# Performance work log

Hardware: AMD Instinct MI355X
Metric: run time of the kernel (lower is better)

Reference implementation:

```python
import jax, jax.numpy as jnp
import numpy as np

H = 128  # hidden_size

def _band_agg(h):
    # Equivalent to bmm(adj, h) with adj = degree-normalized tridiagonal
    # (self + left + right neighbor), degree=3 interior, 2 at endpoints,
    # normalization adj/(deg+1e-8) as in the torch module.
    B, S, D = h.shape
    hp = jnp.pad(h, ((0, 0), (1, 1), (0, 0)))
    s = hp[:, :-2] + hp[:, 1:-1] + hp[:, 2:]            # [B,S,D] neighbor sum
    deg = jnp.full((S,), 3.0, dtype=h.dtype).at[0].set(2.0).at[S - 1].set(2.0)
    return s / (deg + 1e-8)[None, :, None]


def setup_inputs() -> dict:
    key = jax.random.key(0)
    ks = jax.random.split(key, 16)
    f32 = jnp.float32
    p = lambda k, shp: (jax.random.normal(k, shp, dtype=f32) * 0.05)
    return {
        "x": jax.random.normal(ks[0], (32, 2048, 6), dtype=f32),
        "enc_w1": p(ks[1], (6, H)),   "enc_b1": p(ks[2], (H,)),
        "enc_w2": p(ks[3], (H, H)),   "enc_b2": p(ks[4], (H,)),
        "gc1_w": p(ks[5], (H, H)),    "gc1_b": p(ks[6], (H,)),
        "gc2_w": p(ks[7], (H, H)),    "gc2_b": p(ks[8], (H,)),
        "gc3_w": p(ks[9], (H, H)),    "gc3_b": p(ks[10], (H,)),
        "cls_w1": p(ks[11], (H, H // 2)), "cls_b1": p(ks[12], (H // 2,)),
        "cls_w2": p(ks[13], (H // 2, 3)), "cls_b2": p(ks[14], (3,)),
    }


def reference(x, enc_w1, enc_b1, enc_w2, enc_b2,
              gc1_w, gc1_b, gc2_w, gc2_b, gc3_w, gc3_b,
              cls_w1, cls_b1, cls_w2, cls_b2):
    # node encoder: Linear -> ReLU -> Linear
    h = jax.nn.relu(x @ enc_w1 + enc_b1) @ enc_w2 + enc_b2
    # three graph convolutions: linear, normalized tridiagonal aggregate, relu
    h = jax.nn.relu(_band_agg(h @ gc1_w + gc1_b))
    h = jax.nn.relu(_band_agg(h @ gc2_w + gc2_b))
    h = jax.nn.relu(_band_agg(h @ gc3_w + gc3_b))
    # AdaptiveAvgPool1d(1) over seq dim after transpose == mean over nodes
    pooled = h.mean(axis=1)                              # [B, H]
    # classifier (dropout inactive in eval)
    return jax.nn.relu(pooled @ cls_w1 + cls_b1) @ cls_w2 + cls_b2
```

## Files before the change

### kernel.cpp

```cpp
#include <hip/hip_runtime.h>

#define SEQ  2048
#define HID  128
#define NB   32
#define TILE 58
#define GX   36
#define MSTR 67

typedef float f2    __attribute__((ext_vector_type(2)));
typedef float f32x4 __attribute__((ext_vector_type(4)));
typedef short bf16x8 __attribute__((ext_vector_type(8)));
typedef unsigned u32x4 __attribute__((ext_vector_type(4)));

__device__ __forceinline__ void split_bf16(float v, short& h, short& l) {
  unsigned u = __float_as_uint(v);
  unsigned r = (u + 0x7fffu + ((u >> 16) & 1u)) >> 16;
  h = (short)r;
  const float hf = __uint_as_float(r << 16);
  const float lo = v - hf;
  unsigned u2 = __float_as_uint(lo);
  unsigned r2 = (u2 + 0x7fffu + ((u2 >> 16) & 1u)) >> 16;
  l = (short)r2;
}

__device__ __forceinline__ unsigned cvt_pk_bf16(float a, float b) {
  unsigned r;
  asm("v_cvt_pk_bf16_f32 %0, %1, %2" : "=v"(r) : "v"(a), "v"(b));
  return r;
}

__global__ __launch_bounds__(256) void prep_kernel(
    const float* __restrict__ enc_w2, const float* __restrict__ enc_b2,
    const float* __restrict__ gc1_w, const float* __restrict__ gc1_b,
    const float* __restrict__ gc2_w, const float* __restrict__ gc3_w,
    short* __restrict__ Wf, float* __restrict__ bp, unsigned* __restrict__ cnt)
{
  const int tid = threadIdx.x;
  const int bid = blockIdx.x;

  if (bid == 96) {
    if (tid < 128) {
      float s = gc1_b[tid];
      for (int k = 0; k < 128; ++k) s = fmaf(enc_b2[k], gc1_w[k * 128 + tid], s);
      bp[tid] = s;
    }
    if (tid < NB) cnt[tid] = 0u;
    return;
  }

  const int L = bid >> 5, bx = bid & 31;
  short* hi = Wf + L * 32768;
  short* lo = hi + 16384;

  if (L == 0) {
    __shared__ float As[32 * 128];
    __shared__ float Bs[128 * 16];
    const int k0 = (bx >> 3) * 32, n0 = (bx & 7) * 16;
    for (int i = tid; i < 1024; i += 256)
      ((f32x4*)As)[i] = ((const f32x4*)(enc_w2 + k0 * 128))[i];
    for (int i = tid; i < 512; i += 256) {
      const int t = i >> 2, q = i & 3;
      ((f32x4*)Bs)[i] = *(const f32x4*)(gc1_w + t * 128 + n0 + q * 4);
    }
    __syncthreads();
    #pragma unroll
    for (int e = 0; e < 2; ++e) {
      const int f = tid + e * 256;
      const int l = f >> 3, j = f & 7;
      const float* ar = As + ((l >> 4) * 8 + j) * 128;
      const int nn = l & 15;
      float s0 = 0.f, s1 = 0.f, s2 = 0.f, s3 = 0.f;
      for (int t = 0; t < 128; t += 4) {
        s0 = fmaf(ar[t + 0], Bs[(t + 0) * 16 + nn], s0);
        s1 = fmaf(ar[t + 1], Bs[(t + 1) * 16 + nn], s1);
        s2 = fmaf(ar[t + 2], Bs[(t + 2) * 16 + nn], s2);
        s3 = fmaf(ar[t + 3], Bs[(t + 3) * 16 + nn], s3);
      }
      short h, lw;
      split_bf16((s0 + s1) + (s2 + s3), h, lw);
      hi[bx * 512 + f] = h; lo[bx * 512 + f] = lw;
    }
  } else {
    const float* __restrict__ SW = (L == 1) ? gc2_w : gc3_w;
    const int ks = bx >> 3, nt = bx & 7;
    for (int f = tid; f < 512; f += 256) {
      const int l = f >> 3, j = f & 7;
      const int k = ks * 32 + (l >> 4) * 8 + j;
      const int n = nt * 16 + (l & 15);
      short h, lw;
      split_bf16(SW[k * 128 + n], h, lw);
      hi[bx * 512 + f] = h; lo[bx * 512 + f] = lw;
    }
  }
}

__global__ __launch_bounds__(256) void fused_kernel(
    const float* __restrict__ x,
    const float* __restrict__ enc_w1, const float* __restrict__ enc_b1,
    const short* __restrict__ Wf, const float* __restrict__ bp,
    const float* __restrict__ gc2_b, const float* __restrict__ gc3_b,
    float* __restrict__ partial, unsigned* __restrict__ cnt,
    const float* __restrict__ cls_w1, const float* __restrict__ cls_b1,
    const float* __restrict__ cls_w2, const float* __restrict__ cls_b2,
    float* __restrict__ out)
{
  __shared__ float hT[HID * MSTR];
  __shared__ float wsmall[7 * HID];
  __shared__ float psum[256];
  __shared__ int lastf;

  const int tid  = threadIdx.x;
  const int lane = tid & 63;
  const int w    = tid >> 6;
  const int gxb  = blockIdx.x, b = blockIdx.y;
  const int s0   = gxb * TILE;

  for (int f = tid; f < 7 * HID; f += 256)
    wsmall[f] = (f < 6 * HID) ? enc_w1[f] : enc_b1[f - 6 * HID];

  const int sm = s0 - 3 + lane;
  float xv[6];
  if (sm >= 0 && sm < SEQ) {
    const f2* xp = (const f2*)(x + ((long long)b * SEQ + sm) * 6);
    const f2 a0 = xp[0], a1 = xp[1], a2 = xp[2];
    xv[0] = a0.x; xv[1] = a0.y; xv[2] = a1.x;
    xv[3] = a1.y; xv[4] = a2.x; xv[5] = a2.y;
  } else {
    #pragma unroll
    for (int k = 0; k < 6; ++k) xv[k] = 0.f;
  }
  __syncthreads();
  {
    const int c0 = w * 32;
    float4 a4[8];
    #pragma unroll
    for (int q = 0; q < 8; ++q) a4[q] = make_float4(0.f, 0.f, 0.f, 0.f);
    #pragma unroll
    for (int k = 0; k < 6; ++k) {
      #pragma unroll
      for (int q = 0; q < 8; ++q) {
        const float4 wv = *(const float4*)&wsmall[k * HID + c0 + q * 4];
        a4[q].x = fmaf(xv[k], wv.x, a4[q].x);
        a4[q].y = fmaf(xv[k], wv.y, a4[q].y);
        a4[q].z = fmaf(xv[k], wv.z, a4[q].z);
        a4[q].w = fmaf(xv[k], wv.w, a4[q].w);
      }
    }
    #pragma unroll
    for (int q = 0; q < 8; ++q) {
      const float4 bb = *(const float4*)&wsmall[6 * HID + c0 + q * 4];
      const int c = c0 + q * 4;
      hT[(c + 0) * MSTR + lane] = fmaxf(a4[q].x + bb.x, 0.f);
      hT[(c + 1) * MSTR + lane] = fmaxf(a4[q].y + bb.y, 0.f);
      hT[(c + 2) * MSTR + lane] = fmaxf(a4[q].z + bb.z, 0.f);
      hT[(c + 3) * MSTR + lane] = fmaxf(a4[q].w + bb.w, 0.f);
    }
  }
  __syncthreads();

  const int mt   = w * 16 + (lane & 15);
  const int koct = (lane >> 4) * 8;
  const int stt  = s0 - 3 + mt;
  const float invdA = (stt == 0 || stt == SEQ - 1) ? (1.0f / (2.0f + 1e-8f))
                                                   : (1.0f / (3.0f + 1e-8f));
  const int mm = (mt == 0) ? 0 : mt - 1;
  const int mp = (mt == 63) ? 63 : mt + 1;

  #pragma unroll 1
  for (int L = 0; L < 3; ++L) {
    const short* WfL = Wf + L * 32768;
    const bf16x8* Bhi = (const bf16x8*)WfL;
    const bf16x8* Blo = (const bf16x8*)(WfL + 16384);
    const float* bias = (L == 0) ? bp : (L == 1) ? gc2_b : gc3_b;

    f32x4 acc_[8];
    #pragma unroll
    for (int nt = 0; nt < 8; ++nt) acc_[nt] = (f32x4){0.f, 0.f, 0.f, 0.f};

    #pragma unroll 1
    for (int ks = 0; ks < 4; ++ks) {
      const int fb = ks * 512 + lane;
      bf16x8 bh[8], bl[8];
      #pragma unroll
      for (int nt = 0; nt < 8; ++nt) {
        bh[nt] = Bhi[fb + nt * 64];
        bl[nt] = Blo[fb + nt * 64];
      }
      bf16x8 ah, al;
      {
        const float* pa = &hT[(ks * 32 + koct) * MSTR];
        float v[8];
        #pragma unroll
        for (int j = 0; j < 8; ++j) {
          if (L == 0) {
            v[j] = pa[j * MSTR + mt];
          } else {
            const float t = (pa[j * MSTR + mm] + pa[j * MSTR + mt] +
                             pa[j * MSTR + mp]) * invdA;
            v[j] = fmaxf(t, 0.f);
          }
        }
        u32x4 hv, lv;
        #pragma unroll
        for (int q = 0; q < 4; ++q) {
          const unsigned hp = cvt_pk_bf16(v[2 * q], v[2 * q + 1]);
          const float h0 = __uint_as_float(hp << 16);
          const float h1 = __uint_as_float(hp & 0xffff0000u);
          hv[q] = hp;
          lv[q] = cvt_pk_bf16(v[2 * q] - h0, v[2 * q + 1] - h1);
        }
        ah = __builtin_bit_cast(bf16x8, hv);
        al = __builtin_bit_cast(bf16x8, lv);
      }
      #pragma unroll
      for (int nt = 0; nt < 8; ++nt) {
        acc_[nt] = __builtin_amdgcn_mfma_f32_16x16x32_bf16(ah, bh[nt], acc_[nt], 0, 0, 0);
        acc_[nt] = __builtin_amdgcn_mfma_f32_16x16x32_bf16(ah, bl[nt], acc_[nt], 0, 0, 0);
        acc_[nt] = __builtin_amdgcn_mfma_f32_16x16x32_bf16(al, bh[nt], acc_[nt], 0, 0, 0);
      }
    }
    __syncthreads();

    {
      const int n0 = lane & 15;
      const int mrow0 = w * 16 + (lane >> 4) * 4;
      #pragma unroll
      for (int nt = 0; nt < 8; ++nt) {
        const float bn = bias[nt * 16 + n0];
        float* pw = &hT[(nt * 16 + n0) * MSTR];
        #pragma unroll
        for (int r = 0; r < 4; ++r) {
          const int m = mrow0 + r;
          const int s = s0 - 3 + m;
          const bool vld = (s >= 0 && s < SEQ);
          pw[m] = vld ? (acc_[nt][r] + bn) : 0.f;
        }
      }
    }
    __syncthreads();
  }

  {
    const int c = tid & 127, half = tid >> 7;
    float ps = 0.f;
    const float* pc = &hT[c * MSTR];
    #pragma unroll 1
    for (int r = 0; r < 29; ++r) {
      const int m = 3 + half * 29 + r;
      const int s = s0 + half * 29 + r;
      if (s < SEQ) {
        const float invd = (s == 0 || s == SEQ - 1) ? (1.0f / (2.0f + 1e-8f))
                                                    : (1.0f / (3.0f + 1e-8f));
        ps += fmaxf((pc[m - 1] + pc[m] + pc[m + 1]) * invd, 0.f);
      }
    }
    psum[tid] = ps;
  }
  __syncthreads();

  if (tid < 128) {
    __hip_atomic_store(&partial[((long long)b * GX + gxb) * HID + tid],
                       psum[tid] + psum[tid + 128],
                       __ATOMIC_RELAXED, __HIP_MEMORY_SCOPE_AGENT);
  }
  asm volatile("s_waitcnt vmcnt(0)" ::: "memory");
  __syncthreads();
  if (tid == 0) {
    const unsigned old = __hip_atomic_fetch_add(&cnt[b], 1u, __ATOMIC_RELAXED,
                                                __HIP_MEMORY_SCOPE_AGENT);
    lastf = (old == GX - 1) ? 1 : 0;
  }
  __syncthreads();
  if (!lastf) return;

  if (tid < 128) {
    float a = 0.f;
    #pragma unroll
    for (int g = 0; g < GX; ++g)
      a += __hip_atomic_load(&partial[((long long)b * GX + g) * HID + tid],
                             __ATOMIC_RELAXED, __HIP_MEMORY_SCOPE_AGENT);
    psum[tid] = a * (1.0f / 2048.0f);
  }
  __syncthreads();
  if (tid < 64) {
    float h = cls_b1[tid];
    for (int k = 0; k < 128; ++k) h = fmaf(psum[k], cls_w1[k * 64 + tid], h);
    psum[128 + tid] = fmaxf(h, 0.f);
  }
  __syncthreads();
  if (tid < 3) {
    float o = cls_b2[tid];
    for (int k = 0; k < 64; ++k) o = fmaf(psum[128 + k], cls_w2[k * 3 + tid], o);
    out[b * 3 + tid] = o;
  }
}

extern "C" void kernel_launch(void* const* d_in, const int* in_sizes, int n_in,
                              void* d_out, int out_size, void* d_ws, size_t ws_size,
                              hipStream_t stream) {
  (void)in_sizes; (void)n_in; (void)out_size; (void)ws_size;
  const float* x      = (const float*)d_in[0];
  const float* enc_w1 = (const float*)d_in[1];
  const float* enc_b1 = (const float*)d_in[2];
  const float* enc_w2 = (const float*)d_in[3];
  const float* enc_b2 = (const float*)d_in[4];
  const float* gc1_w  = (const float*)d_in[5];
  const float* gc1_b  = (const float*)d_in[6];
  const float* gc2_w  = (const float*)d_in[7];
  const float* gc2_b  = (const float*)d_in[8];
  const float* gc3_w  = (const float*)d_in[9];
  const float* gc3_b  = (const float*)d_in[10];
  const float* cls_w1 = (const float*)d_in[11];
  const float* cls_b1 = (const float*)d_in[12];
  const float* cls_w2 = (const float*)d_in[13];
  const float* cls_b2 = (const float*)d_in[14];

  float* bpv     = (float*)d_ws;
  short* Wfrag   = (short*)(bpv + 128);
  float* partial = (float*)(Wfrag + 3 * 2 * 16384);
  unsigned* cntb = (unsigned*)(partial + (long long)NB * GX * HID);

  prep_kernel<<<dim3(97), 256, 0, stream>>>(enc_w2, enc_b2, gc1_w, gc1_b,
                                            gc2_w, gc3_w, Wfrag, bpv, cntb);
  fused_kernel<<<dim3(GX, NB), 256, 0, stream>>>(
      x, enc_w1, enc_b1, Wfrag, bpv, gc2_b, gc3_b, partial, cntb,
      cls_w1, cls_b1, cls_w2, cls_b2, (float*)d_out);
}
```

Before: 137.1 us.

## Double block size to 512 threads, splitting output columns across wave groups

Launches the fused kernel with 512 threads (8 waves) instead of 256. Each wave now computes 16 rows by 64 output columns, so per-wave accumulators and B-fragment registers are halved, and the encoder and pooling loops are spread across more threads. The aim is more waves in flight per CU to hide global weight loads and LDS latency, at the cost of each A-fragment being built twice (once per column half) and more barrier participants.

```diff
diff --git a/kernel.cpp b/kernel.cpp
--- a/kernel.cpp
+++ b/kernel.cpp
@@ -94,7 +94,7 @@
   }
 }
 
-__global__ __launch_bounds__(256) void fused_kernel(
+__global__ __launch_bounds__(512, 6) void fused_kernel(
     const float* __restrict__ x,
     const float* __restrict__ enc_w1, const float* __restrict__ enc_b1,
     const short* __restrict__ Wf, const float* __restrict__ bp,
@@ -106,16 +106,19 @@
 {
   __shared__ float hT[HID * MSTR];
   __shared__ float wsmall[7 * HID];
-  __shared__ float psum[256];
+  __shared__ float psum[512];
   __shared__ int lastf;
 
   const int tid  = threadIdx.x;
   const int lane = tid & 63;
-  const int w    = tid >> 6;
+  const int w8   = tid >> 6;
+  const int wm   = w8 & 3;
+  const int wg   = w8 >> 2;
   const int gxb  = blockIdx.x, b = blockIdx.y;
   const int s0   = gxb * TILE;
-
-  for (int f = tid; f < 7 * HID; f += 256)
+  const bf16x8* Bf = (const bf16x8*)Wf;
+
+  for (int f = tid; f < 7 * HID; f += 512)
     wsmall[f] = (f < 6 * HID) ? enc_w1[f] : enc_b1[f - 6 * HID];
 
   const int sm = s0 - 3 + lane;
@@ -131,14 +134,14 @@
   }
   __syncthreads();
   {
-    const int c0 = w * 32;
-    float4 a4[8];
-    #pragma unroll
-    for (int q = 0; q < 8; ++q) a4[q] = make_float4(0.f, 0.f, 0.f, 0.f);
+    const int c0 = w8 * 16;
+    float4 a4[4];
+    #pragma unroll
+    for (int q = 0; q < 4; ++q) a4[q] = make_float4(0.f, 0.f, 0.f, 0.f);
     #pragma unroll
     for (int k = 0; k < 6; ++k) {
       #pragma unroll
-      for (int q = 0; q < 8; ++q) {
+      for (int q = 0; q < 4; ++q) {
         const float4 wv = *(const float4*)&wsmall[k * HID + c0 + q * 4];
         a4[q].x = fmaf(xv[k], wv.x, a4[q].x);
         a4[q].y = fmaf(xv[k], wv.y, a4[q].y);
@@ -147,7 +150,7 @@
       }
     }
     #pragma unroll
-    for (int q = 0; q < 8; ++q) {
+    for (int q = 0; q < 4; ++q) {
       const float4 bb = *(const float4*)&wsmall[6 * HID + c0 + q * 4];
       const int c = c0 + q * 4;
       hT[(c + 0) * MSTR + lane] = fmaxf(a4[q].x + bb.x, 0.f);
@@ -158,8 +161,9 @@
   }
   __syncthreads();
 
-  const int mt   = w * 16 + (lane & 15);
+  const int mt   = wm * 16 + (lane & 15);
   const int koct = (lane >> 4) * 8;
+  const int ntb  = wg * 4;
   const int stt  = s0 - 3 + mt;
   const float invdA = (stt == 0 || stt == SEQ - 1) ? (1.0f / (2.0f + 1e-8f))
                                                    : (1.0f / (3.0f + 1e-8f));
@@ -168,23 +172,22 @@
 
   #pragma unroll 1
   for (int L = 0; L < 3; ++L) {
-    const short* WfL = Wf + L * 32768;
-    const bf16x8* Bhi = (const bf16x8*)WfL;
-    const bf16x8* Blo = (const bf16x8*)(WfL + 16384);
+    const bf16x8* BhL = Bf + L * 4096;
+    const bf16x8* BlL = BhL + 2048;
     const float* bias = (L == 0) ? bp : (L == 1) ? gc2_b : gc3_b;
 
-    f32x4 acc_[8];
-    #pragma unroll
-    for (int nt = 0; nt < 8; ++nt) acc_[nt] = (f32x4){0.f, 0.f, 0.f, 0.f};
+    f32x4 acc_[4];
+    #pragma unroll
+    for (int i = 0; i < 4; ++i) acc_[i] = (f32x4){0.f, 0.f, 0.f, 0.f};
 
     #pragma unroll 1
     for (int ks = 0; ks < 4; ++ks) {
-      const int fb = ks * 512 + lane;
-      bf16x8 bh[8], bl[8];
+      const int fb = ks * 512 + ntb * 64 + lane;
+      bf16x8 bh[4], bl[4];
       #pragma unroll
-      for (int nt = 0; nt < 8; ++nt) {
-        bh[nt] = Bhi[fb + nt * 64];
-        bl[nt] = Blo[fb + nt * 64];
+      for (int i = 0; i < 4; ++i) {
+        bh[i] = BhL[fb + i * 64];
+        bl[i] = BlL[fb + i * 64];
       }
       bf16x8 ah, al;
       {
@@ -213,27 +216,28 @@
         al = __builtin_bit_cast(bf16x8, lv);
       }
       #pragma unroll
-      for (int nt = 0; nt < 8; ++nt) {
-        acc_[nt] = __builtin_amdgcn_mfma_f32_16x16x32_bf16(ah, bh[nt], acc_[nt], 0, 0, 0);
-        acc_[nt] = __builtin_amdgcn_mfma_f32_16x16x32_bf16(ah, bl[nt], acc_[nt], 0, 0, 0);
-        acc_[nt] = __builtin_amdgcn_mfma_f32_16x16x32_bf16(al, bh[nt], acc_[nt], 0, 0, 0);
+      for (int i = 0; i < 4; ++i) {
+        acc_[i] = __builtin_amdgcn_mfma_f32_16x16x32_bf16(ah, bh[i], acc_[i], 0, 0, 0);
+        acc_[i] = __builtin_amdgcn_mfma_f32_16x16x32_bf16(ah, bl[i], acc_[i], 0, 0, 0);
+        acc_[i] = __builtin_amdgcn_mfma_f32_16x16x32_bf16(al, bh[i], acc_[i], 0, 0, 0);
       }
     }
     __syncthreads();
 
     {
       const int n0 = lane & 15;
-      const int mrow0 = w * 16 + (lane >> 4) * 4;
+      const int mrow0 = wm * 16 + (lane >> 4) * 4;
       #pragma unroll
-      for (int nt = 0; nt < 8; ++nt) {
-        const float bn = bias[nt * 16 + n0];
-        float* pw = &hT[(nt * 16 + n0) * MSTR];
+      for (int i = 0; i < 4; ++i) {
+        const int n = (ntb + i) * 16 + n0;
+        const float bn = bias[n];
+        float* pw = &hT[n * MSTR];
         #pragma unroll
         for (int r = 0; r < 4; ++r) {
           const int m = mrow0 + r;
           const int s = s0 - 3 + m;
           const bool vld = (s >= 0 && s < SEQ);
-          pw[m] = vld ? (acc_[nt][r] + bn) : 0.f;
+          pw[m] = vld ? (acc_[i][r] + bn) : 0.f;
         }
       }
     }
@@ -241,13 +245,13 @@
   }
 
   {
-    const int c = tid & 127, half = tid >> 7;
+    const int c = tid & 127, q4 = tid >> 7;
     float ps = 0.f;
     const float* pc = &hT[c * MSTR];
     #pragma unroll 1
-    for (int r = 0; r < 29; ++r) {
-      const int m = 3 + half * 29 + r;
-      const int s = s0 + half * 29 + r;
+    for (int r = q4; r < TILE; r += 4) {
+      const int m = 3 + r;
+      const int s = s0 + r;
       if (s < SEQ) {
         const float invd = (s == 0 || s == SEQ - 1) ? (1.0f / (2.0f + 1e-8f))
                                                     : (1.0f / (3.0f + 1e-8f));
@@ -260,7 +264,7 @@
 
   if (tid < 128) {
     __hip_atomic_store(&partial[((long long)b * GX + gxb) * HID + tid],
-                       psum[tid] + psum[tid + 128],
+                       psum[tid] + psum[tid + 128] + psum[tid + 256] + psum[tid + 384],
                        __ATOMIC_RELAXED, __HIP_MEMORY_SCOPE_AGENT);
   }
   asm volatile("s_waitcnt vmcnt(0)" ::: "memory");
@@ -322,7 +326,7 @@
 
   prep_kernel<<<dim3(97), 256, 0, stream>>>(enc_w2, enc_b2, gc1_w, gc1_b,
                                             gc2_w, gc3_w, Wfrag, bpv, cntb);
-  fused_kernel<<<dim3(GX, NB), 256, 0, stream>>>(
+  fused_kernel<<<dim3(GX, NB), 512, 0, stream>>>(
       x, enc_w1, enc_b1, Wfrag, bpv, gc2_b, gc3_b, partial, cntb,
       cls_w1, cls_b1, cls_w2, cls_b2, (float*)d_out);
 }
```

Result: no change. 138.8 us (+1.2%).

## Enlarge sequence tile to 96 rows with 6-wave blocks to cut halo overhead

Applied to the files above, without the earlier changes.

Raises the per-block tile from 64 to 96 rows (86 useful plus halo) using 384 threads, cutting the grid from 36 to 24 blocks per batch. This shrinks the share of redundant halo recompute across the three graph-conv layers. The first-layer encoder is rewritten to stage x in shared memory and compute per-channel with weights held in registers. The larger LDS footprint and launch bound of 5 waves may limit occupancy.

```diff
diff --git a/kernel.cpp b/kernel.cpp
--- a/kernel.cpp
+++ b/kernel.cpp
@@ -3,9 +3,10 @@
 #define SEQ  2048
 #define HID  128
 #define NB   32
-#define TILE 58
-#define GX   36
-#define MSTR 67
+#define TILE 86
+#define GX   24
+#define MROWS 96
+#define MSTR 97
 
 typedef float f2    __attribute__((ext_vector_type(2)));
 typedef float f32x4 __attribute__((ext_vector_type(4)));
@@ -94,7 +95,7 @@
   }
 }
 
-__global__ __launch_bounds__(256) void fused_kernel(
+__global__ __launch_bounds__(384, 5) void fused_kernel(
     const float* __restrict__ x,
     const float* __restrict__ enc_w1, const float* __restrict__ enc_b1,
     const short* __restrict__ Wf, const float* __restrict__ bp,
@@ -105,8 +106,7 @@
     float* __restrict__ out)
 {
   __shared__ float hT[HID * MSTR];
-  __shared__ float wsmall[7 * HID];
-  __shared__ float psum[256];
+  __shared__ float xsps[576];
   __shared__ int lastf;
 
   const int tid  = threadIdx.x;
@@ -114,46 +114,32 @@
   const int w    = tid >> 6;
   const int gxb  = blockIdx.x, b = blockIdx.y;
   const int s0   = gxb * TILE;
-
-  for (int f = tid; f < 7 * HID; f += 256)
-    wsmall[f] = (f < 6 * HID) ? enc_w1[f] : enc_b1[f - 6 * HID];
-
-  const int sm = s0 - 3 + lane;
-  float xv[6];
-  if (sm >= 0 && sm < SEQ) {
-    const f2* xp = (const f2*)(x + ((long long)b * SEQ + sm) * 6);
-    const f2 a0 = xp[0], a1 = xp[1], a2 = xp[2];
-    xv[0] = a0.x; xv[1] = a0.y; xv[2] = a1.x;
-    xv[3] = a1.y; xv[4] = a2.x; xv[5] = a2.y;
-  } else {
+  const bf16x8* Bf = (const bf16x8*)Wf;
+
+  for (int i = tid; i < 288; i += 384) {
+    const int row = i / 3, p = i - row * 3;
+    const int s = s0 - 3 + row;
+    f2 v = {0.f, 0.f};
+    if (s >= 0 && s < SEQ)
+      v = *(const f2*)(x + ((long long)b * SEQ + s) * 6 + p * 2);
+    ((f2*)xsps)[i] = v;
+  }
+  __syncthreads();
+
+  {
+    const int c = tid & 127, g = tid >> 7;
+    float w1r[6];
     #pragma unroll
-    for (int k = 0; k < 6; ++k) xv[k] = 0.f;
-  }
-  __syncthreads();
-  {
-    const int c0 = w * 32;
-    float4 a4[8];
-    #pragma unroll
-    for (int q = 0; q < 8; ++q) a4[q] = make_float4(0.f, 0.f, 0.f, 0.f);
-    #pragma unroll
-    for (int k = 0; k < 6; ++k) {
+    for (int k = 0; k < 6; ++k) w1r[k] = enc_w1[k * HID + c];
+    const float b1r = enc_b1[c];
+    #pragma unroll 4
+    for (int r = 0; r < 32; ++r) {
+      const int m = g * 32 + r;
+      const float* xr = &xsps[m * 6];
+      float a = b1r;
       #pragma unroll
-      for (int q = 0; q < 8; ++q) {
-        const float4 wv = *(const float4*)&wsmall[k * HID + c0 + q * 4];
-        a4[q].x = fmaf(xv[k], wv.x, a4[q].x);
-        a4[q].y = fmaf(xv[k], wv.y, a4[q].y);
-        a4[q].z = fmaf(xv[k], wv.z, a4[q].z);
-        a4[q].w = fmaf(xv[k], wv.w, a4[q].w);
-      }
-    }
-    #pragma unroll
-    for (int q = 0; q < 8; ++q) {
-      const float4 bb = *(const float4*)&wsmall[6 * HID + c0 + q * 4];
-      const int c = c0 + q * 4;
-      hT[(c + 0) * MSTR + lane] = fmaxf(a4[q].x + bb.x, 0.f);
-      hT[(c + 1) * MSTR + lane] = fmaxf(a4[q].y + bb.y, 0.f);
-      hT[(c + 2) * MSTR + lane] = fmaxf(a4[q].z + bb.z, 0.f);
-      hT[(c + 3) * MSTR + lane] = fmaxf(a4[q].w + bb.w, 0.f);
+      for (int k = 0; k < 6; ++k) a = fmaf(xr[k], w1r[k], a);
+      hT[c * MSTR + m] = fmaxf(a, 0.f);
     }
   }
   __syncthreads();
@@ -164,13 +150,12 @@
   const float invdA = (stt == 0 || stt == SEQ - 1) ? (1.0f / (2.0f + 1e-8f))
                                                    : (1.0f / (3.0f + 1e-8f));
   const int mm = (mt == 0) ? 0 : mt - 1;
-  const int mp = (mt == 63) ? 63 : mt + 1;
+  const int mp = (mt == MROWS - 1) ? (MROWS - 1) : mt + 1;
 
   #pragma unroll 1
   for (int L = 0; L < 3; ++L) {
-    const short* WfL = Wf + L * 32768;
-    const bf16x8* Bhi = (const bf16x8*)WfL;
-    const bf16x8* Blo = (const bf16x8*)(WfL + 16384);
+    const bf16x8* BhL = Bf + L * 4096;
+    const bf16x8* BlL = BhL + 2048;
     const float* bias = (L == 0) ? bp : (L == 1) ? gc2_b : gc3_b;
 
     f32x4 acc_[8];
@@ -183,8 +168,8 @@
       bf16x8 bh[8], bl[8];
       #pragma unroll
       for (int nt = 0; nt < 8; ++nt) {
-        bh[nt] = Bhi[fb + nt * 64];
-        bl[nt] = Blo[fb + nt * 64];
+        bh[nt] = BhL[fb + nt * 64];
+        bl[nt] = BlL[fb + nt * 64];
       }
       bf16x8 ah, al;
       {
@@ -241,26 +226,26 @@
   }
 
   {
-    const int c = tid & 127, half = tid >> 7;
+    const int c = tid & 127, q = tid >> 7;
     float ps = 0.f;
     const float* pc = &hT[c * MSTR];
     #pragma unroll 1
-    for (int r = 0; r < 29; ++r) {
-      const int m = 3 + half * 29 + r;
-      const int s = s0 + half * 29 + r;
+    for (int r = q; r < TILE; r += 3) {
+      const int m = 3 + r;
+      const int s = s0 + r;
       if (s < SEQ) {
         const float invd = (s == 0 || s == SEQ - 1) ? (1.0f / (2.0f + 1e-8f))
                                                     : (1.0f / (3.0f + 1e-8f));
         ps += fmaxf((pc[m - 1] + pc[m] + pc[m + 1]) * invd, 0.f);
       }
     }
-    psum[tid] = ps;
+    xsps[tid] = ps;
   }
   __syncthreads();
 
   if (tid < 128) {
     __hip_atomic_store(&partial[((long long)b * GX + gxb) * HID + tid],
-                       psum[tid] + psum[tid + 128],
+                       xsps[tid] + xsps[tid + 128] + xsps[tid + 256],
                        __ATOMIC_RELAXED, __HIP_MEMORY_SCOPE_AGENT);
   }
   asm volatile("s_waitcnt vmcnt(0)" ::: "memory");
@@ -279,18 +264,18 @@
     for (int g = 0; g < GX; ++g)
       a += __hip_atomic_load(&partial[((long long)b * GX + g) * HID + tid],
                              __ATOMIC_RELAXED, __HIP_MEMORY_SCOPE_AGENT);
-    psum[tid] = a * (1.0f / 2048.0f);
+    xsps[tid] = a * (1.0f / 2048.0f);
   }
   __syncthreads();
   if (tid < 64) {
     float h = cls_b1[tid];
-    for (int k = 0; k < 128; ++k) h = fmaf(psum[k], cls_w1[k * 64 + tid], h);
-    psum[128 + tid] = fmaxf(h, 0.f);
+    for (int k = 0; k < 128; ++k) h = fmaf(xsps[k], cls_w1[k * 64 + tid], h);
+    xsps[128 + tid] = fmaxf(h, 0.f);
   }
   __syncthreads();
   if (tid < 3) {
     float o = cls_b2[tid];
-    for (int k = 0; k < 64; ++k) o = fmaf(psum[128 + k], cls_w2[k * 3 + tid], o);
+    for (int k = 0; k < 64; ++k) o = fmaf(xsps[128 + k], cls_w2[k * 3 + tid], o);
     out[b * 3 + tid] = o;
   }
 }
@@ -322,7 +307,7 @@
 
   prep_kernel<<<dim3(97), 256, 0, stream>>>(enc_w2, enc_b2, gc1_w, gc1_b,
                                             gc2_w, gc3_w, Wfrag, bpv, cntb);
-  fused_kernel<<<dim3(GX, NB), 256, 0, stream>>>(
+  fused_kernel<<<dim3(GX, NB), 384, 0, stream>>>(
       x, enc_w1, enc_b1, Wfrag, bpv, gc2_b, gc3_b, partial, cntb,
       cls_w1, cls_b1, cls_w2, cls_b2, (float*)d_out);
 }
```

Measured after the change: 228.0 us. +66.2%, slower.
